# Kernel optimization log

Hardware: AMD Instinct MI355X
Metric: run time of the kernel (lower is better)

Reference implementation:

```python
import jax, jax.numpy as jnp
import numpy as np

N = 100000
E = 1600000
IN_C = 256
HID = 128
OUT_C = 128
HEADS = 4
C_HEAD = HID // HEADS
BN_EPS = 1e-5
NEG_SLOPE = 0.2


def setup_inputs() -> dict:
    key = jax.random.key(0)
    ks = jax.random.split(key, 12)
    s = lambda fan: 1.0 / np.sqrt(fan)
    return {
        "x": jax.random.normal(ks[0], (N, IN_C), dtype=jnp.float32),
        "W_gat": jax.random.normal(ks[1], (IN_C, HID), dtype=jnp.float32) * s(IN_C),
        "att_src": jax.random.normal(ks[2], (HEADS, C_HEAD), dtype=jnp.float32) * s(C_HEAD),
        "att_dst": jax.random.normal(ks[3], (HEADS, C_HEAD), dtype=jnp.float32) * s(C_HEAD),
        "bias_gat": jnp.zeros((HID,), dtype=jnp.float32),
        "bn1_gamma": jnp.ones((HID,), dtype=jnp.float32),
        "bn1_beta": jnp.zeros((HID,), dtype=jnp.float32),
        "eps_gin": jnp.zeros((), dtype=jnp.float32),
        "lin_W": jax.random.normal(ks[4], (HID, OUT_C), dtype=jnp.float32) * s(HID),
        "lin_b": jnp.zeros((OUT_C,), dtype=jnp.float32),
        "bn2_gamma": jnp.ones((OUT_C,), dtype=jnp.float32),
        "bn2_beta": jnp.zeros((OUT_C,), dtype=jnp.float32),
        "edge_index": jax.random.randint(ks[5], (2, E), 0, N, dtype=jnp.int64),
    }


def batch_norm(h, gamma, beta):
    mu = jnp.mean(h, axis=0)
    var = jnp.var(h, axis=0)
    return (h - mu) * jax.lax.rsqrt(var + BN_EPS) * gamma + beta


def reference(x, W_gat, att_src, att_dst, bias_gat, bn1_gamma, bn1_beta,
              eps_gin, lin_W, lin_b, bn2_gamma, bn2_beta, edge_index):
    src, dst = edge_index[0], edge_index[1]
    # ---- GATConv ----
    h = (x @ W_gat).reshape(N, HEADS, C_HEAD)              # [N,H,C]
    a_src = jnp.einsum('nhc,hc->nh', h, att_src)            # [N,H]
    a_dst = jnp.einsum('nhc,hc->nh', h, att_dst)            # [N,H]
    e = jax.nn.leaky_relu(a_src[src] + a_dst[dst], NEG_SLOPE)  # [E,H]
    # segment softmax over incoming edges of each dst node
    m = jax.ops.segment_max(e, dst, num_segments=N)         # [N,H]
    num = jnp.exp(e - m[dst])                                # [E,H]
    den = jax.ops.segment_sum(num, dst, num_segments=N)      # [N,H]
    alpha = num / den[dst]                                   # [E,H]
    msg = alpha[:, :, None] * h[src]                         # [E,H,C]
    out1 = jax.ops.segment_sum(msg, dst, num_segments=N)     # [N,H,C]
    out1 = out1.reshape(N, HID) + bias_gat
    # BN + ELU (dropout = identity in eval)
    out1 = jax.nn.elu(batch_norm(out1, bn1_gamma, bn1_beta))
    # ---- GINConv: nn((1+eps)*x + sum_neighbors) ----
    agg = jax.ops.segment_sum(out1[src], dst, num_segments=N)
    z = (1.0 + eps_gin) * out1 + agg
    out2 = z @ lin_W + lin_b
    out2 = jax.nn.elu(batch_norm(out2, bn2_gamma, bn2_beta))
    return out2
```

## Files before the change

kernel.cpp:

```cpp
#include <hip/hip_runtime.h>

#define N_NODES 100000
#define N_EDGES 1600000
#define IN_C 256
#define HID 128
#define NEG_SLOPE 0.2f
#define BN_EPS 1e-5f
#define NBUCK 391
#define NPART 391
#define GAT_BLOCKS 2048

typedef unsigned int uint32;
typedef __attribute__((ext_vector_type(8))) short bf16x8;
typedef __attribute__((ext_vector_type(4))) float f32x4;

__device__ __forceinline__ float lrelu(float x) { return x > 0.f ? x : NEG_SLOPE * x; }

__device__ __forceinline__ unsigned short f2bf(float f) {
    uint32 u = __float_as_uint(f);
    u += 0x7fffu + ((u >> 16) & 1u);
    return (unsigned short)(u >> 16);
}
__device__ __forceinline__ float bf2f(unsigned short h) {
    return __uint_as_float(((uint32)h) << 16);
}
__device__ __forceinline__ float bflo(uint32 v) { return __uint_as_float(v << 16); }
__device__ __forceinline__ float bfhi(uint32 v) { return __uint_as_float(v & 0xffff0000u); }
__device__ __forceinline__ uint32 packbf(float a, float b) {
    return (uint32)f2bf(a) | ((uint32)f2bf(b) << 16);
}

__global__ void k_init(int* __restrict__ bcount, float* __restrict__ bnacc) {
    int t = threadIdx.x;
    if (t < NBUCK) bcount[t] = 0;
    if (t < 512) bnacc[t] = 0.f;
}

__global__ void k_transpose_all(const float* __restrict__ W1, const float* __restrict__ W2,
                                unsigned short* __restrict__ Wt1,
                                unsigned short* __restrict__ Wt2) {
    int idx = blockIdx.x * 256 + threadIdx.x;
    if (idx < IN_C * 128) {
        int k = idx >> 7, n = idx & 127;
        Wt1[n * IN_C + k] = f2bf(W1[idx]);
    } else {
        idx -= IN_C * 128;
        if (idx < HID * 128) {
            int k = idx >> 7, n = idx & 127;
            Wt2[n * HID + k] = f2bf(W2[idx]);
        }
    }
}

template <bool AF32, bool OUTF32, bool ATT, bool STATS>
__global__ __launch_bounds__(256) void k_gemm(const void* __restrict__ Av,
                                              const unsigned short* __restrict__ Wt,
                                              void* __restrict__ Out, int K,
                                              const float* __restrict__ att_s,
                                              const float* __restrict__ att_d,
                                              float* __restrict__ a_src,
                                              float* __restrict__ a_dst,
                                              float* __restrict__ bnst) {
    __shared__ unsigned short As[128 * 72];
    __shared__ unsigned short Bs[128 * 72];
    const int t = threadIdx.x;
    const int n0 = blockIdx.x * 128;
    const int wv = t >> 6, lane = t & 63;
    const int wy = wv >> 1, wx = wv & 1;
    const int lm = lane & 15, lg = lane >> 4;
    const float* Af = (const float*)Av;
    const unsigned short* Ah = (const unsigned short*)Av;

    f32x4 acc[4][4];
#pragma unroll
    for (int i = 0; i < 4; ++i)
#pragma unroll
        for (int j = 0; j < 4; ++j) acc[i][j] = (f32x4){0.f, 0.f, 0.f, 0.f};

    float4 afp[8];
    uint4 ahp[4];
    uint4 bvp[4];

    if (AF32) {
#pragma unroll
        for (int p = 0; p < 8; ++p) {
            int idx = p * 256 + t, row = idx >> 4, c4 = idx & 15, gn = n0 + row;
            afp[p] = (gn < N_NODES) ? *(const float4*)&Af[(size_t)gn * K + c4 * 4]
                                    : make_float4(0.f, 0.f, 0.f, 0.f);
        }
    } else {
#pragma unroll
        for (int p = 0; p < 4; ++p) {
            int idx = p * 256 + t, row = idx >> 3, c = idx & 7, gn = n0 + row;
            ahp[p] = (gn < N_NODES) ? *(const uint4*)&Ah[(size_t)gn * K + c * 8]
                                    : make_uint4(0, 0, 0, 0);
        }
    }
#pragma unroll
    for (int p = 0; p < 4; ++p) {
        int idx = p * 256 + t, n = idx >> 3, c = idx & 7;
        bvp[p] = *(const uint4*)&Wt[(size_t)n * K + c * 8];
    }

    for (int kc = 0; kc < K; kc += 64) {
        if (AF32) {
#pragma unroll
            for (int p = 0; p < 8; ++p) {
                int idx = p * 256 + t, row = idx >> 4, c4 = idx & 15;
                ushort4 b;
                b.x = f2bf(afp[p].x); b.y = f2bf(afp[p].y);
                b.z = f2bf(afp[p].z); b.w = f2bf(afp[p].w);
                *(ushort4*)&As[row * 72 + c4 * 4] = b;
            }
        } else {
#pragma unroll
            for (int p = 0; p < 4; ++p) {
                int idx = p * 256 + t, row = idx >> 3, c = idx & 7;
                *(uint4*)&As[row * 72 + c * 8] = ahp[p];
            }
        }
#pragma unroll
        for (int p = 0; p < 4; ++p) {
            int idx = p * 256 + t, n = idx >> 3, c = idx & 7;
            *(uint4*)&Bs[n * 72 + c * 8] = bvp[p];
        }
        __syncthreads();
        int kn = kc + 64;
        if (kn < K) {
            if (AF32) {
#pragma unroll
                for (int p = 0; p < 8; ++p) {
                    int idx = p * 256 + t, row = idx >> 4, c4 = idx & 15, gn = n0 + row;
                    afp[p] = (gn < N_NODES) ? *(const float4*)&Af[(size_t)gn * K + kn + c4 * 4]
                                            : make_float4(0.f, 0.f, 0.f, 0.f);
                }
            } else {
#pragma unroll
                for (int p = 0; p < 4; ++p) {
                    int idx = p * 256 + t, row = idx >> 3, c = idx & 7, gn = n0 + row;
                    ahp[p] = (gn < N_NODES) ? *(const uint4*)&Ah[(size_t)gn * K + kn + c * 8]
                                            : make_uint4(0, 0, 0, 0);
                }
            }
#pragma unroll
            for (int p = 0; p < 4; ++p) {
                int idx = p * 256 + t, n = idx >> 3, c = idx & 7;
                bvp[p] = *(const uint4*)&Wt[(size_t)n * K + kn + c * 8];
            }
        }
#pragma unroll
        for (int ks = 0; ks < 2; ++ks) {
            bf16x8 af[4], bfr[4];
#pragma unroll
            for (int i = 0; i < 4; ++i)
                af[i] = *(const bf16x8*)&As[(wy * 64 + i * 16 + lm) * 72 + ks * 32 + lg * 8];
#pragma unroll
            for (int j = 0; j < 4; ++j)
                bfr[j] = *(const bf16x8*)&Bs[(wx * 64 + j * 16 + lm) * 72 + ks * 32 + lg * 8];
#pragma unroll
            for (int i = 0; i < 4; ++i)
#pragma unroll
                for (int j = 0; j < 4; ++j)
                    acc[i][j] = __builtin_amdgcn_mfma_f32_16x16x32_bf16(af[i], bfr[j],
                                                                        acc[i][j], 0, 0, 0);
        }
        __syncthreads();
    }

    float as_w[4], ad_w[4];
    if (ATT) {
#pragma unroll
        for (int j = 0; j < 4; ++j) {
            int col = wx * 64 + j * 16 + lm;
            as_w[j] = att_s[col];
            ad_w[j] = att_d[col];
        }
    }
    float ls[4] = {0.f, 0.f, 0.f, 0.f}, lq[4] = {0.f, 0.f, 0.f, 0.f};
#pragma unroll
    for (int i = 0; i < 4; ++i) {
#pragma unroll
        for (int r = 0; r < 4; ++r) {
            int row = n0 + wy * 64 + i * 16 + lg * 4 + r;
            float v0 = acc[i][0][r], v1 = acc[i][1][r];
            float v2 = acc[i][2][r], v3 = acc[i][3][r];
            if (row < N_NODES) {
                if (OUTF32) {
                    float* op = (float*)Out + (size_t)row * 128 + wx * 64 + lm;
                    op[0] = v0; op[16] = v1; op[32] = v2; op[48] = v3;
                } else {
                    unsigned short* op =
                        (unsigned short*)Out + (size_t)row * 128 + wx * 64 + lm;
                    op[0] = f2bf(v0); op[16] = f2bf(v1);
                    op[32] = f2bf(v2); op[48] = f2bf(v3);
                }
            }
            if (STATS) {
                ls[0] += v0; lq[0] += v0 * v0;
                ls[1] += v1; lq[1] += v1 * v1;
                ls[2] += v2; lq[2] += v2 * v2;
                ls[3] += v3; lq[3] += v3 * v3;
            }
            if (ATT) {
                float ps0 = v0 * as_w[0] + v1 * as_w[1];
                float ps1 = v2 * as_w[2] + v3 * as_w[3];
                float pd0 = v0 * ad_w[0] + v1 * ad_w[1];
                float pd1 = v2 * ad_w[2] + v3 * ad_w[3];
#pragma unroll
                for (int m = 1; m < 16; m <<= 1) {
                    ps0 += __shfl_xor(ps0, m); ps1 += __shfl_xor(ps1, m);
                    pd0 += __shfl_xor(pd0, m); pd1 += __shfl_xor(pd1, m);
                }
                if (lm == 0 && row < N_NODES) {
                    *(float2*)&a_src[row * 4 + wx * 2] = make_float2(ps0, ps1);
                    *(float2*)&a_dst[row * 4 + wx * 2] = make_float2(pd0, pd1);
                }
            }
        }
    }
    if (STATS) {
#pragma unroll
        for (int j = 0; j < 4; ++j) {
            float s = ls[j], q = lq[j];
            s += __shfl_xor(s, 16); s += __shfl_xor(s, 32);
            q += __shfl_xor(q, 16); q += __shfl_xor(q, 32);
            if (lg == 0) {
                int col = wx * 64 + j * 16 + lm;
                atomicAdd(&bnst[col], s);
                atomicAdd(&bnst[128 + col], q);
            }
        }
    }
}

__global__ __launch_bounds__(256) void k_bucket_count(const int* __restrict__ ei,
                                                      int* __restrict__ bcount) {
    __shared__ int hist[NBUCK];
    for (int i = threadIdx.x; i < NBUCK; i += 256) hist[i] = 0;
    __syncthreads();
    for (int e = blockIdx.x * 256 + threadIdx.x; e < N_EDGES; e += gridDim.x * 256)
        atomicAdd(&hist[ei[N_EDGES + e] >> 8], 1);
    __syncthreads();
    for (int i = threadIdx.x; i < NBUCK; i += 256)
        if (hist[i]) atomicAdd(&bcount[i], hist[i]);
}

__global__ void k_bucket_scan(const int* __restrict__ bcount, int* __restrict__ bucket_base,
                              int* __restrict__ gcursor, int* __restrict__ row_ptr) {
    __shared__ int sh[512];
    int t = threadIdx.x;
    int v0 = (t < NBUCK) ? bcount[t] : 0;
    int val = v0;
    sh[t] = val;
    __syncthreads();
    for (int off = 1; off < 512; off <<= 1) {
        int o = (t >= off) ? sh[t - off] : 0;
        __syncthreads();
        val += o;
        sh[t] = val;
        __syncthreads();
    }
    if (t < NBUCK) {
        int e = val - v0;
        bucket_base[t] = e;
        gcursor[t] = e;
    }
    if (t == 0) {
        bucket_base[NBUCK] = N_EDGES;
        row_ptr[N_NODES] = N_EDGES;
    }
}

__global__ __launch_bounds__(256) void k_partition(const int* __restrict__ ei,
                                                   int* __restrict__ gcursor,
                                                   int* __restrict__ staging) {
    __shared__ int hist[NBUCK];
    __shared__ int base[NBUCK];
    int t = threadIdx.x;
    int e0 = blockIdx.x * 4096;
    for (int i = t; i < NBUCK; i += 256) hist[i] = 0;
    __syncthreads();
    int pk[16], cb[16];
#pragma unroll
    for (int u = 0; u < 16; ++u) {
        int e = e0 + u * 256 + t;
        cb[u] = -1;
        if (e < N_EDGES) {
            int s = ei[e], d = ei[N_EDGES + e];
            int b = d >> 8;
            int r = atomicAdd(&hist[b], 1);
            pk[u] = ((d & 255) << 17) | s;
            cb[u] = (r << 9) | b;
        }
    }
    __syncthreads();
    for (int i = t; i < NBUCK; i += 256)
        if (hist[i]) base[i] = atomicAdd(&gcursor[i], hist[i]);
    __syncthreads();
#pragma unroll
    for (int u = 0; u < 16; ++u) {
        if (cb[u] >= 0) {
            int b = cb[u] & 511, r = cb[u] >> 9;
            staging[base[b] + r] = pk[u];
        }
    }
}

__global__ __launch_bounds__(256) void k_bucket_sort(const int* __restrict__ staging,
                                                     const int* __restrict__ bucket_base,
                                                     int* __restrict__ row_ptr,
                                                     int* __restrict__ sorted_src) {
    __shared__ int hist[256];
    __shared__ int sh[256];
    int t = threadIdx.x, b = blockIdx.x;
    int lo = bucket_base[b], hi = bucket_base[b + 1];
    hist[t] = 0;
    __syncthreads();
    for (int i = lo + t; i < hi; i += 256) atomicAdd(&hist[staging[i] >> 17], 1);
    __syncthreads();
    int v0 = hist[t];
    int val = v0;
    sh[t] = val;
    __syncthreads();
    for (int off = 1; off < 256; off <<= 1) {
        int o = (t >= off) ? sh[t - off] : 0;
        __syncthreads();
        val += o;
        sh[t] = val;
        __syncthreads();
    }
    int excl = val - v0;
    int d = b * 256 + t;
    if (d < N_NODES) row_ptr[d] = lo + excl;
    hist[t] = excl;
    __syncthreads();
    for (int i = lo + t; i < hi; i += 256) {
        int p = staging[i];
        int r = atomicAdd(&hist[p >> 17], 1);
        sorted_src[lo + r] = p & 0x1FFFF;
    }
}

__global__ __launch_bounds__(256) void k_gat_agg(const uint32* __restrict__ h32,
                                                 const float* __restrict__ a_src,
                                                 const float* __restrict__ a_dst,
                                                 const int* __restrict__ row_ptr,
                                                 const int* __restrict__ sorted_src,
                                                 uint32* __restrict__ out1,
                                                 float* __restrict__ bnacc) {
    __shared__ alignas(16) float wbuf[4][4][72];
    __shared__ float sred[4][64][4];
    int lane = threadIdx.x & 63, wv = threadIdx.x >> 6;
    int hd = lane >> 4;
    float s0 = 0.f, s1 = 0.f, q0 = 0.f, q1 = 0.f;
    for (int node = blockIdx.x * 4 + wv; node < N_NODES; node += GAT_BLOCKS * 4) {
        int start = row_ptr[node];
        int deg = row_ptr[node + 1] - start;
        if (deg == 0) {
            out1[((uint32)node << 6) + lane] = 0u;
            continue;
        }
        float4 ad = *(const float4*)&a_dst[node * 4];
        float acc0 = 0.f, acc1 = 0.f, den = 0.f;
        for (int j0 = 0; j0 < deg; j0 += 64) {
            int m = min(64, deg - j0);
            int s = 0;
            float4 w = make_float4(0.f, 0.f, 0.f, 0.f);
            if (lane < m) {
                s = sorted_src[start + j0 + lane];
                float4 as = *(const float4*)&a_src[s * 4];
                w.x = __expf(lrelu(as.x + ad.x));
                w.y = __expf(lrelu(as.y + ad.y));
                w.z = __expf(lrelu(as.z + ad.z));
                w.w = __expf(lrelu(as.w + ad.w));
            }
            wbuf[wv][0][lane] = w.x;
            wbuf[wv][1][lane] = w.y;
            wbuf[wv][2][lane] = w.z;
            wbuf[wv][3][lane] = w.w;
            __builtin_amdgcn_wave_barrier();
            int e0 = 0;
            for (; e0 + 8 <= m; e0 += 8) {
                uint32 hr[8];
#pragma unroll
                for (int k = 0; k < 8; ++k) {
                    int ss = __builtin_amdgcn_readlane(s, e0 + k);
                    hr[k] = h32[((uint32)ss << 6) + lane];
                }
                float4 w0 = *(const float4*)&wbuf[wv][hd][e0];
                float4 w1 = *(const float4*)&wbuf[wv][hd][e0 + 4];
                float wk[8] = {w0.x, w0.y, w0.z, w0.w, w1.x, w1.y, w1.z, w1.w};
#pragma unroll
                for (int k = 0; k < 8; ++k) {
                    den += wk[k];
                    acc0 = fmaf(wk[k], bflo(hr[k]), acc0);
                    acc1 = fmaf(wk[k], bfhi(hr[k]), acc1);
                }
            }
            for (; e0 < m; ++e0) {
                int ss = __builtin_amdgcn_readlane(s, e0);
                uint32 hv = h32[((uint32)ss << 6) + lane];
                float wk = wbuf[wv][hd][e0];
                den += wk;
                acc0 = fmaf(wk, bflo(hv), acc0);
                acc1 = fmaf(wk, bfhi(hv), acc1);
            }
            __builtin_amdgcn_wave_barrier();
        }
        float rden = 1.f / den;
        float o0 = acc0 * rden, o1 = acc1 * rden;
        s0 += o0; q0 += o0 * o0;
        s1 += o1; q1 += o1 * o1;
        out1[((uint32)node << 6) + lane] = packbf(o0, o1);
    }
    sred[wv][lane][0] = s0; sred[wv][lane][1] = s1;
    sred[wv][lane][2] = q0; sred[wv][lane][3] = q1;
    __syncthreads();
    if (wv == 0) {
#pragma unroll
        for (int g = 1; g < 4; ++g) {
            s0 += sred[g][lane][0]; s1 += sred[g][lane][1];
            q0 += sred[g][lane][2]; q1 += sred[g][lane][3];
        }
        int c0 = lane * 2;
        atomicAdd(&bnacc[c0], s0);
        atomicAdd(&bnacc[c0 + 1], s1);
        atomicAdd(&bnacc[128 + c0], q0);
        atomicAdd(&bnacc[128 + c0 + 1], q1);
    }
}

__global__ __launch_bounds__(256) void k_gin_agg(const uint32* __restrict__ ob,
                                                 const int* __restrict__ row_ptr,
                                                 const int* __restrict__ sorted_src,
                                                 const float* __restrict__ eps_ptr,
                                                 uint32* __restrict__ zb) {
    int lane = threadIdx.x & 63, wv = threadIdx.x >> 6;
    int node = blockIdx.x * 4 + wv;
    int start = row_ptr[node];
    int deg = row_ptr[node + 1] - start;
    float acc0 = 0.f, acc1 = 0.f;
    for (int j0 = 0; j0 < deg; j0 += 64) {
        int m = min(64, deg - j0);
        int s = 0;
        if (lane < m) s = sorted_src[start + j0 + lane];
        int e0 = 0;
        for (; e0 + 8 <= m; e0 += 8) {
            uint32 hr[8];
#pragma unroll
            for (int k = 0; k < 8; ++k) {
                int ss = __builtin_amdgcn_readlane(s, e0 + k);
                hr[k] = ob[((uint32)ss << 6) + lane];
            }
#pragma unroll
            for (int k = 0; k < 8; ++k) {
                acc0 += bflo(hr[k]);
                acc1 += bfhi(hr[k]);
            }
        }
        for (; e0 < m; ++e0) {
            int ss = __builtin_amdgcn_readlane(s, e0);
            uint32 hv = ob[((uint32)ss << 6) + lane];
            acc0 += bflo(hv);
            acc1 += bfhi(hv);
        }
    }
    float ep = 1.f + eps_ptr[0];
    uint32 own = ob[((uint32)node << 6) + lane];
    zb[((uint32)node << 6) + lane] = packbf(fmaf(ep, bflo(own), acc0),
                                            fmaf(ep, bfhi(own), acc1));
}

__global__ __launch_bounds__(256) void k_bn_elu_b16(uint32* __restrict__ buf,
                                                    const float* __restrict__ acc,
                                                    const float* __restrict__ gamma,
                                                    const float* __restrict__ beta) {
    __shared__ float psc[128], psh[128];
    int t = threadIdx.x;
    if (t < 128) {
        float mu = acc[t] * (1.f / N_NODES);
        float var = acc[128 + t] * (1.f / N_NODES) - mu * mu;
        float s = rsqrtf(var + BN_EPS) * gamma[t];
        psc[t] = s;
        psh[t] = beta[t] - mu * s;
    }
    __syncthreads();
    size_t i = (size_t)blockIdx.x * 256 + t;
    if (i >= (size_t)N_NODES * 64) return;
    int c0 = (int)(i & 63) * 2;
    uint32 v = buf[i];
    float r0 = fmaf(bflo(v), psc[c0], psh[c0]);
    float r1 = fmaf(bfhi(v), psc[c0 + 1], psh[c0 + 1]);
    r0 = r0 > 0.f ? r0 : __expf(r0) - 1.f;
    r1 = r1 > 0.f ? r1 : __expf(r1) - 1.f;
    buf[i] = packbf(r0, r1);
}

__global__ __launch_bounds__(256) void k_bn_elu_out(const uint32* __restrict__ in,
                                                    const float* __restrict__ acc,
                                                    const float* __restrict__ gamma,
                                                    const float* __restrict__ beta,
                                                    float2* __restrict__ out) {
    __shared__ float psc[128], psh[128];
    int t = threadIdx.x;
    if (t < 128) {
        float mu = acc[t] * (1.f / N_NODES);
        float var = acc[128 + t] * (1.f / N_NODES) - mu * mu;
        float s = rsqrtf(var + BN_EPS) * gamma[t];
        psc[t] = s;
        psh[t] = beta[t] - mu * s;
    }
    __syncthreads();
    size_t i = (size_t)blockIdx.x * 256 + t;
    if (i >= (size_t)N_NODES * 64) return;
    int c0 = (int)(i & 63) * 2;
    uint32 v = in[i];
    float r0 = fmaf(bflo(v), psc[c0], psh[c0]);
    float r1 = fmaf(bfhi(v), psc[c0 + 1], psh[c0 + 1]);
    r0 = r0 > 0.f ? r0 : __expf(r0) - 1.f;
    r1 = r1 > 0.f ? r1 : __expf(r1) - 1.f;
    out[i] = make_float2(r0, r1);
}

extern "C" void kernel_launch(void* const* d_in, const int* in_sizes, int n_in,
                              void* d_out, int out_size, void* d_ws, size_t ws_size,
                              hipStream_t stream) {
    (void)in_sizes; (void)n_in; (void)out_size; (void)ws_size;
    const float* x       = (const float*)d_in[0];
    const float* W_gat   = (const float*)d_in[1];
    const float* att_src = (const float*)d_in[2];
    const float* att_dst = (const float*)d_in[3];
    const float* bn1_g   = (const float*)d_in[5];
    const float* bn1_b   = (const float*)d_in[6];
    const float* eps_gin = (const float*)d_in[7];
    const float* lin_W   = (const float*)d_in[8];
    const float* bn2_g   = (const float*)d_in[10];
    const float* bn2_b   = (const float*)d_in[11];
    const int*   ei      = (const int*)d_in[12];
    float* out = (float*)d_out;

    char* w = (char*)d_ws;
    size_t o = 0;
    auto take = [&](size_t b) -> char* {
        char* p = w + o;
        o += (b + 255) & ~(size_t)255;
        return p;
    };
    unsigned short* hb   = (unsigned short*)take((size_t)N_NODES * 128 * 2);
    unsigned short* Wt1  = (unsigned short*)take((size_t)128 * IN_C * 2);
    unsigned short* Wt2  = (unsigned short*)take((size_t)128 * HID * 2);
    uint32* o1b          = (uint32*)take((size_t)N_NODES * 64 * 4);
    float* a_src         = (float*)take((size_t)N_NODES * 4 * 4);
    float* a_dst         = (float*)take((size_t)N_NODES * 4 * 4);
    int*   sorted        = (int*)take((size_t)N_EDGES * 4);
    int*   staging       = (int*)take((size_t)N_EDGES * 4);
    int*   row_ptr       = (int*)take((size_t)(N_NODES + 1) * 4);
    int*   bcount        = (int*)take((NBUCK + 1) * 4);
    int*   bucket_base   = (int*)take((NBUCK + 1) * 4);
    int*   gcursor       = (int*)take((NBUCK + 1) * 4);
    float* bnacc         = (float*)take(512 * 4);
    uint32* zb  = (uint32*)hb;
    uint32* o2b = o1b;

    const int nGemmBlocks = (N_NODES + 127) / 128;
    const int nElemBlocks = (N_NODES * 64 + 255) / 256;

    k_init<<<1, 512, 0, stream>>>(bcount, bnacc);
    k_transpose_all<<<((IN_C + HID) * 128 + 255) / 256, 256, 0, stream>>>(W_gat, lin_W,
                                                                          Wt1, Wt2);
    k_gemm<true, false, true, false><<<nGemmBlocks, 256, 0, stream>>>(
        x, Wt1, hb, IN_C, att_src, att_dst, a_src, a_dst, nullptr);
    k_bucket_count<<<256, 256, 0, stream>>>(ei, bcount);
    k_bucket_scan<<<1, 512, 0, stream>>>(bcount, bucket_base, gcursor, row_ptr);
    k_partition<<<NPART, 256, 0, stream>>>(ei, gcursor, staging);
    k_bucket_sort<<<NBUCK, 256, 0, stream>>>(staging, bucket_base, row_ptr, sorted);
    k_gat_agg<<<GAT_BLOCKS, 256, 0, stream>>>((const uint32*)hb, a_src, a_dst, row_ptr,
                                              sorted, o1b, bnacc);
    k_bn_elu_b16<<<nElemBlocks, 256, 0, stream>>>(o1b, bnacc, bn1_g, bn1_b);
    k_gin_agg<<<N_NODES / 4, 256, 0, stream>>>(o1b, row_ptr, sorted, eps_gin, zb);
    k_gemm<false, false, false, true><<<nGemmBlocks, 256, 0, stream>>>(
        zb, Wt2, o2b, HID, nullptr, nullptr, nullptr, nullptr, bnacc + 256);
    k_bn_elu_out<<<nElemBlocks, 256, 0, stream>>>(o2b, bnacc + 256, bn2_g, bn2_b,
                                                  (float2*)out);
}
```

Before: 576.9 us.

## Launch one wave per node in GAT aggregation and split out BN statistics

```diff
diff --git a/kernel.cpp b/kernel.cpp
--- a/kernel.cpp
+++ b/kernel.cpp
@@ -8,7 +8,6 @@
 #define BN_EPS 1e-5f
 #define NBUCK 391
 #define NPART 391
-#define GAT_BLOCKS 2048
 
 typedef unsigned int uint32;
 typedef __attribute__((ext_vector_type(8))) short bf16x8;
@@ -346,88 +345,66 @@
                                                  const float* __restrict__ a_dst,
                                                  const int* __restrict__ row_ptr,
                                                  const int* __restrict__ sorted_src,
-                                                 uint32* __restrict__ out1,
-                                                 float* __restrict__ bnacc) {
+                                                 uint32* __restrict__ out1) {
     __shared__ alignas(16) float wbuf[4][4][72];
-    __shared__ float sred[4][64][4];
     int lane = threadIdx.x & 63, wv = threadIdx.x >> 6;
     int hd = lane >> 4;
-    float s0 = 0.f, s1 = 0.f, q0 = 0.f, q1 = 0.f;
-    for (int node = blockIdx.x * 4 + wv; node < N_NODES; node += GAT_BLOCKS * 4) {
-        int start = row_ptr[node];
-        int deg = row_ptr[node + 1] - start;
-        if (deg == 0) {
-            out1[((uint32)node << 6) + lane] = 0u;
-            continue;
-        }
-        float4 ad = *(const float4*)&a_dst[node * 4];
-        float acc0 = 0.f, acc1 = 0.f, den = 0.f;
-        for (int j0 = 0; j0 < deg; j0 += 64) {
-            int m = min(64, deg - j0);
-            int s = 0;
-            float4 w = make_float4(0.f, 0.f, 0.f, 0.f);
-            if (lane < m) {
-                s = sorted_src[start + j0 + lane];
-                float4 as = *(const float4*)&a_src[s * 4];
-                w.x = __expf(lrelu(as.x + ad.x));
-                w.y = __expf(lrelu(as.y + ad.y));
-                w.z = __expf(lrelu(as.z + ad.z));
-                w.w = __expf(lrelu(as.w + ad.w));
-            }
-            wbuf[wv][0][lane] = w.x;
-            wbuf[wv][1][lane] = w.y;
-            wbuf[wv][2][lane] = w.z;
-            wbuf[wv][3][lane] = w.w;
-            __builtin_amdgcn_wave_barrier();
-            int e0 = 0;
-            for (; e0 + 8 <= m; e0 += 8) {
-                uint32 hr[8];
-#pragma unroll
-                for (int k = 0; k < 8; ++k) {
-                    int ss = __builtin_amdgcn_readlane(s, e0 + k);
-                    hr[k] = h32[((uint32)ss << 6) + lane];
-                }
-                float4 w0 = *(const float4*)&wbuf[wv][hd][e0];
-                float4 w1 = *(const float4*)&wbuf[wv][hd][e0 + 4];
-                float wk[8] = {w0.x, w0.y, w0.z, w0.w, w1.x, w1.y, w1.z, w1.w};
-#pragma unroll
-                for (int k = 0; k < 8; ++k) {
-                    den += wk[k];
-                    acc0 = fmaf(wk[k], bflo(hr[k]), acc0);
-                    acc1 = fmaf(wk[k], bfhi(hr[k]), acc1);
-                }
-            }
-            for (; e0 < m; ++e0) {
-                int ss = __builtin_amdgcn_readlane(s, e0);
-                uint32 hv = h32[((uint32)ss << 6) + lane];
-                float wk = wbuf[wv][hd][e0];
-                den += wk;
-                acc0 = fmaf(wk, bflo(hv), acc0);
-                acc1 = fmaf(wk, bfhi(hv), acc1);
-            }
-            __builtin_amdgcn_wave_barrier();
-        }
-        float rden = 1.f / den;
-        float o0 = acc0 * rden, o1 = acc1 * rden;
-        s0 += o0; q0 += o0 * o0;
-        s1 += o1; q1 += o1 * o1;
-        out1[((uint32)node << 6) + lane] = packbf(o0, o1);
-    }
-    sred[wv][lane][0] = s0; sred[wv][lane][1] = s1;
-    sred[wv][lane][2] = q0; sred[wv][lane][3] = q1;
-    __syncthreads();
-    if (wv == 0) {
-#pragma unroll
-        for (int g = 1; g < 4; ++g) {
-            s0 += sred[g][lane][0]; s1 += sred[g][lane][1];
-            q0 += sred[g][lane][2]; q1 += sred[g][lane][3];
-        }
-        int c0 = lane * 2;
-        atomicAdd(&bnacc[c0], s0);
-        atomicAdd(&bnacc[c0 + 1], s1);
-        atomicAdd(&bnacc[128 + c0], q0);
-        atomicAdd(&bnacc[128 + c0 + 1], q1);
-    }
+    int node = blockIdx.x * 4 + wv;
+    int start = row_ptr[node];
+    int deg = row_ptr[node + 1] - start;
+    if (deg == 0) {
+        out1[((uint32)node << 6) + lane] = 0u;
+        return;
+    }
+    float4 ad = *(const float4*)&a_dst[node * 4];
+    float acc0 = 0.f, acc1 = 0.f, den = 0.f;
+    for (int j0 = 0; j0 < deg; j0 += 64) {
+        int m = min(64, deg - j0);
+        int s = 0;
+        float4 w = make_float4(0.f, 0.f, 0.f, 0.f);
+        if (lane < m) {
+            s = sorted_src[start + j0 + lane];
+            float4 as = *(const float4*)&a_src[s * 4];
+            w.x = __expf(lrelu(as.x + ad.x));
+            w.y = __expf(lrelu(as.y + ad.y));
+            w.z = __expf(lrelu(as.z + ad.z));
+            w.w = __expf(lrelu(as.w + ad.w));
+        }
+        wbuf[wv][0][lane] = w.x;
+        wbuf[wv][1][lane] = w.y;
+        wbuf[wv][2][lane] = w.z;
+        wbuf[wv][3][lane] = w.w;
+        __builtin_amdgcn_wave_barrier();
+        int e0 = 0;
+        for (; e0 + 8 <= m; e0 += 8) {
+            uint32 hr[8];
+#pragma unroll
+            for (int k = 0; k < 8; ++k) {
+                int ss = __builtin_amdgcn_readlane(s, e0 + k);
+                hr[k] = h32[((uint32)ss << 6) + lane];
+            }
+            float4 w0 = *(const float4*)&wbuf[wv][hd][e0];
+            float4 w1 = *(const float4*)&wbuf[wv][hd][e0 + 4];
+            float wk[8] = {w0.x, w0.y, w0.z, w0.w, w1.x, w1.y, w1.z, w1.w};
+#pragma unroll
+            for (int k = 0; k < 8; ++k) {
+                den += wk[k];
+                acc0 = fmaf(wk[k], bflo(hr[k]), acc0);
+                acc1 = fmaf(wk[k], bfhi(hr[k]), acc1);
+            }
+        }
+        for (; e0 < m; ++e0) {
+            int ss = __builtin_amdgcn_readlane(s, e0);
+            uint32 hv = h32[((uint32)ss << 6) + lane];
+            float wk = wbuf[wv][hd][e0];
+            den += wk;
+            acc0 = fmaf(wk, bflo(hv), acc0);
+            acc1 = fmaf(wk, bfhi(hv), acc1);
+        }
+        __builtin_amdgcn_wave_barrier();
+    }
+    float rden = 1.f / den;
+    out1[((uint32)node << 6) + lane] = packbf(acc0 * rden, acc1 * rden);
 }
 
 __global__ __launch_bounds__(256) void k_gin_agg(const uint32* __restrict__ ob,
@@ -469,6 +446,33 @@
     uint32 own = ob[((uint32)node << 6) + lane];
     zb[((uint32)node << 6) + lane] = packbf(fmaf(ep, bflo(own), acc0),
                                             fmaf(ep, bfhi(own), acc1));
+}
+
+__global__ __launch_bounds__(256) void k_bnstats_bf16(const uint32* __restrict__ buf,
+                                                      float* __restrict__ acc) {
+    __shared__ float sh[4][64][4];
+    int lane = threadIdx.x & 63, grp = threadIdx.x >> 6;
+    float s0 = 0.f, s1 = 0.f, q0 = 0.f, q1 = 0.f;
+    for (int r = blockIdx.x * 4 + grp; r < N_NODES; r += gridDim.x * 4) {
+        uint32 v = buf[(size_t)r * 64 + lane];
+        float v0 = bflo(v), v1 = bfhi(v);
+        s0 += v0; s1 += v1; q0 += v0 * v0; q1 += v1 * v1;
+    }
+    sh[grp][lane][0] = s0; sh[grp][lane][1] = s1;
+    sh[grp][lane][2] = q0; sh[grp][lane][3] = q1;
+    __syncthreads();
+    if (grp == 0) {
+#pragma unroll
+        for (int g = 1; g < 4; ++g) {
+            s0 += sh[g][lane][0]; s1 += sh[g][lane][1];
+            q0 += sh[g][lane][2]; q1 += sh[g][lane][3];
+        }
+        int c0 = lane * 2;
+        atomicAdd(&acc[c0], s0);
+        atomicAdd(&acc[c0 + 1], s1);
+        atomicAdd(&acc[128 + c0], q0);
+        atomicAdd(&acc[128 + c0 + 1], q1);
+    }
 }
 
 __global__ __launch_bounds__(256) void k_bn_elu_b16(uint32* __restrict__ buf,
@@ -574,8 +578,9 @@
     k_bucket_scan<<<1, 512, 0, stream>>>(bcount, bucket_base, gcursor, row_ptr);
     k_partition<<<NPART, 256, 0, stream>>>(ei, gcursor, staging);
     k_bucket_sort<<<NBUCK, 256, 0, stream>>>(staging, bucket_base, row_ptr, sorted);
-    k_gat_agg<<<GAT_BLOCKS, 256, 0, stream>>>((const uint32*)hb, a_src, a_dst, row_ptr,
-                                              sorted, o1b, bnacc);
+    k_gat_agg<<<N_NODES / 4, 256, 0, stream>>>((const uint32*)hb, a_src, a_dst, row_ptr,
+                                               sorted, o1b);
+    k_bnstats_bf16<<<512, 256, 0, stream>>>(o1b, bnacc);
     k_bn_elu_b16<<<nElemBlocks, 256, 0, stream>>>(o1b, bnacc, bn1_g, bn1_b);
     k_gin_agg<<<N_NODES / 4, 256, 0, stream>>>(o1b, row_ptr, sorted, eps_gin, zb);
     k_gemm<false, false, false, true><<<nGemmBlocks, 256, 0, stream>>>(
```

After: 522.4 us. 1.1x faster.
